# Performance work log

Hardware: AMD Instinct MI355X
Metric: run time of the kernel (lower is better)

The kernel has to match this reference:

```python
import jax, jax.numpy as jnp
import numpy as np

NUM_HEADS = 16
HIDDEN = 1024
HEAD = HIDDEN // NUM_HEADS


def setup_inputs() -> dict:
    key = jax.random.key(0)
    k1, k2, k3, k4, k5 = jax.random.split(key, 5)
    b, s, d = 2, 2048, HIDDEN
    scale = 1.0 / np.sqrt(d)
    return {
        "features": jax.random.normal(k1, (b, s, d), dtype=jnp.float32),
        "qkv_w": jax.random.normal(k2, (3 * d, d), dtype=jnp.float32) * scale,  # torch Linear weight [out,in]
        "qkv_b": jax.random.normal(k3, (3 * d,), dtype=jnp.float32) * 0.01,
        "out_w": jax.random.normal(k4, (d, d), dtype=jnp.float32) * scale,
        "out_b": jax.random.normal(k5, (d,), dtype=jnp.float32) * 0.01,
        "use_causal_mask": 0,
    }


def reference(features, qkv_w, qkv_b, out_w, out_b, use_causal_mask):
    b, s, d = features.shape
    qkv = features @ qkv_w.T + qkv_b                      # [b,s,3d]
    q, k, v = jnp.split(qkv, 3, axis=-1)
    # [b,s,d] -> [b,h,s,hd]
    def heads(x):
        return x.reshape(b, s, NUM_HEADS, HEAD).transpose(0, 2, 1, 3)
    q, k, v = heads(q), heads(k), heads(v)
    scores = jnp.einsum("bhqd,bhkd->bhqk", q, k) / np.sqrt(HEAD)
    if use_causal_mask:
        mask = jnp.triu(jnp.ones((s, s), dtype=bool), k=1)
        scores = jnp.where(mask, -jnp.inf, scores)
    attn = jax.nn.softmax(scores, axis=-1)
    out = jnp.einsum("bhqk,bhkd->bhqd", attn, v)          # [b,h,s,hd]
    out = out.transpose(0, 2, 1, 3).reshape(b, s, d)
    return out @ out_w.T + out_b
```

## Files before the change

kernel.cpp:

```cpp
#include <hip/hip_runtime.h>
#include <hip/hip_bf16.h>
#include <math.h>

#define BATCH 2
#define SEQ   2048
#define HID   1024
#define NHEAD 16
#define ROWS  (BATCH*SEQ)
#define QK_N  2048
#define VT_N  (BATCH*SEQ)

#define Q_SCALE 0.18033688011112042f

typedef __attribute__((ext_vector_type(8))) short bf16x8;
typedef __attribute__((ext_vector_type(4))) float f32x4;

__device__ __forceinline__ unsigned short f2b(float f) {
    unsigned u = __float_as_uint(f);
    u += 0x7FFF + ((u >> 16) & 1);
    return (unsigned short)(u >> 16);
}
__device__ __forceinline__ unsigned pk2c(float a, float b) {
    __hip_bfloat162 h = __float22bfloat162_rn(float2{a, b});
    union { __hip_bfloat162 h2; unsigned u; } cv; cv.h2 = h;
    return cv.u;
}

#define GLOAD_LDS16(gp, lp) \
    __builtin_amdgcn_global_load_lds((const __attribute__((address_space(1))) void*)(gp), \
                                     (__attribute__((address_space(3))) void*)(lp), 16, 0, 0)

__global__ __launch_bounds__(256)
void cvt_all(const float* __restrict__ a, unsigned short* __restrict__ oa, int na4,
             const float* __restrict__ b, unsigned short* __restrict__ ob, int nb4,
             const float* __restrict__ c, unsigned short* __restrict__ oc, int nc4) {
    const int total = na4 + nb4 + nc4;
    const int stride = gridDim.x * 256;
    for (int i = blockIdx.x * 256 + threadIdx.x; i < total; i += stride) {
        const float* src; unsigned short* dst; int j;
        if (i < na4)            { src = a; dst = oa; j = i; }
        else if (i < na4 + nb4) { src = b; dst = ob; j = i - na4; }
        else                    { src = c; dst = oc; j = i - na4 - nb4; }
        float4 v = reinterpret_cast<const float4*>(src)[j];
        ushort4 o;
        o.x = f2b(v.x); o.y = f2b(v.y); o.z = f2b(v.z); o.w = f2b(v.w);
        reinterpret_cast<ushort4*>(dst)[j] = o;
    }
}

__global__ __launch_bounds__(256)
void proj_fused(const unsigned short* __restrict__ fbf,
                const unsigned short* __restrict__ wbf,
                const float* __restrict__ qkv_b,
                unsigned short* __restrict__ qkbf,
                unsigned short* __restrict__ vtD) {
    __shared__ __align__(16) unsigned short As[128 * 32];
    __shared__ __align__(16) unsigned short Bs[128 * 32];
    const int tid = threadIdx.x;
    const int w = tid >> 6, l = tid & 63;
    const int wm = w >> 1, wn = w & 1;
    const int l15 = l & 15, l4 = l >> 4;

    const int bx = blockIdx.x;
    const bool isQK = bx < 512;
    const unsigned short* A;
    const unsigned short* Bm;
    long row0, col0;
    if (isQK) {
        row0 = (long)(bx >> 4) * 128;
        col0 = (long)(bx & 15) * 128;
        A = fbf;  Bm = wbf;
    } else {
        int r = bx - 512;
        row0 = (long)(r >> 5) * 128;
        col0 = (long)(r & 31) * 128;
        A = wbf + (size_t)2048 * 1024;
        Bm = fbf;
    }

    f32x4 acc[4][4];
    #pragma unroll
    for (int m = 0; m < 4; ++m)
        #pragma unroll
        for (int n = 0; n < 4; ++n) acc[m][n] = (f32x4)0.0f;

    const int lr   = l >> 2;
    const int slot = (l & 3) ^ (lr & 3);

    for (int k0 = 0; k0 < HID; k0 += 32) {
        __syncthreads();
        #pragma unroll
        for (int c = 0; c < 2; ++c) {
            int r = w * 32 + c * 16 + lr;
            GLOAD_LDS16(A  + (row0 + r) * HID + k0 + slot * 8, As + (w * 32 + c * 16) * 32);
            GLOAD_LDS16(Bm + (col0 + r) * HID + k0 + slot * 8, Bs + (w * 32 + c * 16) * 32);
        }
        __syncthreads();

        bf16x8 af[4], bfr[4];
        #pragma unroll
        for (int m = 0; m < 4; ++m) {
            int row = wm * 64 + m * 16 + l15;
            af[m] = *(const bf16x8*)((const char*)As + row * 64 + ((l4 ^ (row & 3)) << 4));
        }
        #pragma unroll
        for (int n = 0; n < 4; ++n) {
            int row = wn * 64 + n * 16 + l15;
            bfr[n] = *(const bf16x8*)((const char*)Bs + row * 64 + ((l4 ^ (row & 3)) << 4));
        }
        #pragma unroll
        for (int m = 0; m < 4; ++m)
            #pragma unroll
            for (int n = 0; n < 4; ++n)
                acc[m][n] = __builtin_amdgcn_mfma_f32_16x16x32_bf16(af[m], bfr[n], acc[m][n], 0, 0, 0);
    }

    #pragma unroll
    for (int m = 0; m < 4; ++m) {
        #pragma unroll
        for (int n = 0; n < 4; ++n) {
            long ccol = col0 + wn * 64 + n * 16 + l15;
            #pragma unroll
            for (int r2 = 0; r2 < 4; ++r2) {
                long crow = row0 + wm * 64 + m * 16 + l4 * 4 + r2;
                if (isQK) {
                    float v = acc[m][n][r2] + qkv_b[ccol];
                    qkbf[crow * QK_N + ccol] = (ccol < 1024) ? f2b(v * Q_SCALE) : f2b(v);
                } else {
                    float v = acc[m][n][r2] + qkv_b[2048 + crow];
                    vtD[crow * VT_N + ccol] = f2b(v);
                }
            }
        }
    }
}

__global__ __launch_bounds__(256)
void gemm_out(const unsigned short* __restrict__ A, const unsigned short* __restrict__ B,
              const float* __restrict__ bias, float* __restrict__ Cout,
              int M, int N, int K) {
    __shared__ __align__(16) unsigned short As[128 * 32];
    __shared__ __align__(16) unsigned short Bs[64 * 32];
    const int tid = threadIdx.x;
    const int w = tid >> 6, l = tid & 63;
    const int wm = w >> 1, wn = w & 1;
    const int l15 = l & 15, l4 = l >> 4;
    const long row0 = (long)blockIdx.y * 128;
    const long col0 = (long)blockIdx.x * 64;

    f32x4 acc[4][2];
    #pragma unroll
    for (int m = 0; m < 4; ++m)
        #pragma unroll
        for (int n = 0; n < 2; ++n) acc[m][n] = (f32x4)0.0f;

    const int lr   = l >> 2;
    const int slot = (l & 3) ^ (lr & 3);

    for (int k0 = 0; k0 < K; k0 += 32) {
        __syncthreads();
        #pragma unroll
        for (int c = 0; c < 2; ++c) {
            int r = w * 32 + c * 16 + lr;
            GLOAD_LDS16(A + (row0 + r) * K + k0 + slot * 8, As + (w * 32 + c * 16) * 32);
        }
        {
            int r = w * 16 + lr;
            GLOAD_LDS16(B + (col0 + r) * K + k0 + slot * 8, Bs + (w * 16) * 32);
        }
        __syncthreads();

        bf16x8 af[4], bfr[2];
        #pragma unroll
        for (int m = 0; m < 4; ++m) {
            int row = wm * 64 + m * 16 + l15;
            af[m] = *(const bf16x8*)((const char*)As + row * 64 + ((l4 ^ (row & 3)) << 4));
        }
        #pragma unroll
        for (int n = 0; n < 2; ++n) {
            int row = wn * 32 + n * 16 + l15;
            bfr[n] = *(const bf16x8*)((const char*)Bs + row * 64 + ((l4 ^ (row & 3)) << 4));
        }
        #pragma unroll
        for (int m = 0; m < 4; ++m)
            #pragma unroll
            for (int n = 0; n < 2; ++n)
                acc[m][n] = __builtin_amdgcn_mfma_f32_16x16x32_bf16(af[m], bfr[n], acc[m][n], 0, 0, 0);
    }

    #pragma unroll
    for (int m = 0; m < 4; ++m) {
        #pragma unroll
        for (int n = 0; n < 2; ++n) {
            long ccol = col0 + wn * 32 + n * 16 + l15;
            float bv = bias[ccol];
            #pragma unroll
            for (int r2 = 0; r2 < 4; ++r2) {
                long crow = row0 + wm * 64 + m * 16 + l4 * 4 + r2;
                Cout[crow * N + ccol] = acc[m][n][r2] + bv;
            }
        }
    }
}

__global__ __launch_bounds__(256, 4)
void attn_mfma(const unsigned short* __restrict__ qk, const unsigned short* __restrict__ vtD,
               unsigned short* __restrict__ attno, const int* __restrict__ use_mask) {
    __shared__ __align__(16) unsigned short Ks [64 * 64];
    __shared__ __align__(16) unsigned short Vts[64 * 64];
    __shared__ __align__(16) unsigned short Ps [4][32 * 40];
    const int tid = threadIdx.x;
    const int w = tid >> 6, l = tid & 63;
    const int l15 = l & 15, l4 = l >> 4;
    const int bid  = blockIdx.x;
    const int orig = (bid & 7) * 128 + (bid >> 3);
    const int qt = orig & 31, bh = orig >> 5;
    const int b = bh >> 4, h = bh & 15;
    const int q0 = qt * 64;
    const int qh = w & 1, kh = w >> 1;
    const int wq0 = q0 + qh * 32;
    const int causal = use_mask[0];
    const int NT = causal ? (qt + 1) : (SEQ / 64);

    bf16x8 qf[2][2];
    #pragma unroll
    for (int m = 0; m < 2; ++m) {
        const unsigned short* qp = qk + (size_t)(b * SEQ + wq0 + m * 16 + l15) * QK_N + h * 64;
        qf[m][0] = *(const bf16x8*)(qp + l4 * 8);
        qf[m][1] = *(const bf16x8*)(qp + 32 + l4 * 8);
    }

    f32x4 o_acc[2][4];
    #pragma unroll
    for (int m = 0; m < 2; ++m)
        #pragma unroll
        for (int n = 0; n < 4; ++n) o_acc[m][n] = (f32x4)0.0f;
    f32x4 l_acc[2] = {(f32x4)0.0f, (f32x4)0.0f};

    bf16x8 ones;
    #pragma unroll
    for (int j = 0; j < 8; ++j) ones[j] = (short)0x3F80;

    const int srow = l >> 3, g = l & 7;
    const int r0   = w * 16 + srow;
    const int wso  = (g ^ srow) << 3;
    unsigned short* pw = Ps[w];

    const unsigned short* kp = qk + (size_t)b * SEQ * QK_N + 1024 + h * 64
                                  + (size_t)r0 * QK_N + g * 8;
    const unsigned short* vp = vtD + (size_t)(h * 64 + r0) * VT_N + b * SEQ + g * 8;

    bf16x8 kreg[2], vreg[2];
    kreg[0] = *(const bf16x8*)(kp);
    kreg[1] = *(const bf16x8*)(kp + 8 * QK_N);
    vreg[0] = *(const bf16x8*)(vp);
    vreg[1] = *(const bf16x8*)(vp + 8 * VT_N);
    kp += (size_t)64 * QK_N;
    vp += 64;

    for (int kt = 0; kt < NT; ++kt) {
        __syncthreads();
        #pragma unroll
        for (int c = 0; c < 2; ++c) {
            *(bf16x8*)(Ks  + (r0 + c * 8) * 64 + wso) = kreg[c];
            *(bf16x8*)(Vts + (r0 + c * 8) * 64 + wso) = vreg[c];
        }
        __syncthreads();

        if (kt + 1 < NT) {
            kreg[0] = *(const bf16x8*)(kp);
            kreg[1] = *(const bf16x8*)(kp + 8 * QK_N);
            vreg[0] = *(const bf16x8*)(vp);
            vreg[1] = *(const bf16x8*)(vp + 8 * VT_N);
            kp += (size_t)64 * QK_N;
            vp += 64;
        }

        f32x4 s_acc[2][2];
        #pragma unroll
        for (int n2 = 0; n2 < 2; ++n2)
            #pragma unroll
            for (int m = 0; m < 2; ++m) s_acc[n2][m] = (f32x4)0.0f;
        __builtin_amdgcn_s_setprio(1);
        #pragma unroll
        for (int ks = 0; ks < 2; ++ks) {
            #pragma unroll
            for (int n2 = 0; n2 < 2; ++n2) {
                int row = kh * 32 + n2 * 16 + l15;
                bf16x8 kf = *(const bf16x8*)((const char*)Ks + row * 128 + (((ks * 4 + l4) ^ (row & 7)) << 4));
                #pragma unroll
                for (int m = 0; m < 2; ++m)
                    s_acc[n2][m] = __builtin_amdgcn_mfma_f32_16x16x32_bf16(kf, qf[m][ks], s_acc[n2][m], 0, 0, 0);
            }
        }
        __builtin_amdgcn_s_setprio(0);

        if (causal) {
            int kk0 = kt * 64 + kh * 32;
            #pragma unroll
            for (int n2 = 0; n2 < 2; ++n2)
                #pragma unroll
                for (int m = 0; m < 2; ++m)
                    #pragma unroll
                    for (int r2 = 0; r2 < 4; ++r2) {
                        int krow = kk0 + n2 * 16 + l4 * 4 + r2;
                        int qcol = wq0 + m * 16 + l15;
                        if (krow > qcol) s_acc[n2][m][r2] = -INFINITY;
                    }
        }

        #pragma unroll
        for (int m = 0; m < 2; ++m) {
            int prow = m * 16 + l15;
            #pragma unroll
            for (int n2 = 0; n2 < 2; ++n2) {
                float p0 = __builtin_amdgcn_exp2f(s_acc[n2][m][0]);
                float p1 = __builtin_amdgcn_exp2f(s_acc[n2][m][1]);
                float p2 = __builtin_amdgcn_exp2f(s_acc[n2][m][2]);
                float p3 = __builtin_amdgcn_exp2f(s_acc[n2][m][3]);
                uint2 pk;
                pk.x = pk2c(p0, p1);
                pk.y = pk2c(p2, p3);
                *(uint2*)((char*)pw + prow * 80 + n2 * 32 + l4 * 8) = pk;
            }
        }

        __builtin_amdgcn_s_setprio(1);
        bf16x8 pf[2];
        #pragma unroll
        for (int m = 0; m < 2; ++m) {
            int prow = m * 16 + l15;
            pf[m] = *(const bf16x8*)((const char*)pw + prow * 80 + l4 * 16);
            l_acc[m] = __builtin_amdgcn_mfma_f32_16x16x32_bf16(pf[m], ones, l_acc[m], 0, 0, 0);
        }
        #pragma unroll
        for (int n = 0; n < 4; ++n) {
            int vrow = n * 16 + l15;
            bf16x8 vf = *(const bf16x8*)((const char*)Vts + vrow * 128 + (((kh * 4 + l4) ^ (vrow & 7)) << 4));
            #pragma unroll
            for (int m = 0; m < 2; ++m)
                o_acc[m][n] = __builtin_amdgcn_mfma_f32_16x16x32_bf16(pf[m], vf, o_acc[m][n], 0, 0, 0);
        }
        __builtin_amdgcn_s_setprio(0);
    }

    __syncthreads();
    float* mq = (float*)(qh ? Vts : Ks);
    float* lb = (float*)&Ps[0][0];
    if (kh == 1) {
        #pragma unroll
        for (int m = 0; m < 2; ++m) {
            #pragma unroll
            for (int r2 = 0; r2 < 4; ++r2) {
                int qr = m * 16 + l4 * 4 + r2;
                #pragma unroll
                for (int n = 0; n < 4; ++n)
                    mq[qr * 64 + n * 16 + l15] = o_acc[m][n][r2];
                if (l15 == 0) lb[qh * 32 + qr] = l_acc[m][r2];
            }
        }
    }
    __syncthreads();
    if (kh == 0) {
        #pragma unroll
        for (int m = 0; m < 2; ++m) {
            #pragma unroll
            for (int r2 = 0; r2 < 4; ++r2) {
                int qr = m * 16 + l4 * 4 + r2;
                float lt = l_acc[m][r2] + lb[qh * 32 + qr];
                float inv = 1.0f / lt;
                size_t orow = (size_t)(b * SEQ + wq0 + qr);
                #pragma unroll
                for (int n = 0; n < 4; ++n) {
                    float o = o_acc[m][n][r2] + mq[qr * 64 + n * 16 + l15];
                    attno[orow * HID + h * 64 + n * 16 + l15] = f2b(o * inv);
                }
            }
        }
    }
}

extern "C" void kernel_launch(void* const* d_in, const int* in_sizes, int n_in,
                              void* d_out, int out_size, void* d_ws, size_t ws_size,
                              hipStream_t stream) {
    const float* features = (const float*)d_in[0];
    const float* qkv_w    = (const float*)d_in[1];
    const float* qkv_b    = (const float*)d_in[2];
    const float* out_w    = (const float*)d_in[3];
    const float* out_b    = (const float*)d_in[4];
    const int*   use_mask = (const int*)d_in[5];

    char* ws = (char*)d_ws;
    unsigned short* fbf     = (unsigned short*)(ws);
    unsigned short* wbf     = (unsigned short*)(ws + 8388608);
    unsigned short* owbf    = (unsigned short*)(ws + 14680064);
    unsigned short* qkbf    = (unsigned short*)(ws + 16777216);
    unsigned short* vtD     = (unsigned short*)(ws + 33554432);
    unsigned short* attnobf = (unsigned short*)(ws + 41943040);

    cvt_all<<<2048, 256, 0, stream>>>(features, fbf, 1048576,
                                      qkv_w, wbf, 786432,
                                      out_w, owbf, 262144);

    proj_fused<<<768, 256, 0, stream>>>(fbf, wbf, qkv_b, qkbf, vtD);

    attn_mfma<<<1024, 256, 0, stream>>>(qkbf, vtD, attnobf, use_mask);

    dim3 g3(HID / 64, ROWS / 128);
    gemm_out<<<g3, 256, 0, stream>>>(attnobf, owbf, out_b, (float*)d_out,
                                     ROWS, HID, HID);
}
```

Measured before the change: 130.5 us.

## Double-buffer LDS tiles in QKV projection GEMM to overlap loads with MFMA

Turns the projection GEMM's single-buffered K loop into a two-stage pipeline. Two LDS buffers per operand are used, and the global-to-LDS load for tile t+2 is issued while tile t is computed. Partial vmcnt waits and explicit barriers fence the stages. The goal is to hide global memory latency behind MFMA work. The cost is double the LDS footprint, which may lower occupancy, and the vmcnt count must exactly match the number of outstanding loads.

Measured after the change: 132.3 us. Within noise of the previous version (+1.4%).

```diff
diff --git a/kernel.cpp b/kernel.cpp
--- a/kernel.cpp
+++ b/kernel.cpp
@@ -54,8 +54,8 @@
                 const float* __restrict__ qkv_b,
                 unsigned short* __restrict__ qkbf,
                 unsigned short* __restrict__ vtD) {
-    __shared__ __align__(16) unsigned short As[128 * 32];
-    __shared__ __align__(16) unsigned short Bs[128 * 32];
+    __shared__ __align__(16) unsigned short As[2][128 * 32];
+    __shared__ __align__(16) unsigned short Bs[2][128 * 32];
     const int tid = threadIdx.x;
     const int w = tid >> 6, l = tid & 63;
     const int wm = w >> 1, wn = w & 1;
@@ -87,33 +87,68 @@
     const int lr   = l >> 2;
     const int slot = (l & 3) ^ (lr & 3);
 
-    for (int k0 = 0; k0 < HID; k0 += 32) {
-        __syncthreads();
-        #pragma unroll
-        for (int c = 0; c < 2; ++c) {
-            int r = w * 32 + c * 16 + lr;
-            GLOAD_LDS16(A  + (row0 + r) * HID + k0 + slot * 8, As + (w * 32 + c * 16) * 32);
-            GLOAD_LDS16(Bm + (col0 + r) * HID + k0 + slot * 8, Bs + (w * 32 + c * 16) * 32);
-        }
-        __syncthreads();
-
-        bf16x8 af[4], bfr[4];
-        #pragma unroll
-        for (int m = 0; m < 4; ++m) {
-            int row = wm * 64 + m * 16 + l15;
-            af[m] = *(const bf16x8*)((const char*)As + row * 64 + ((l4 ^ (row & 3)) << 4));
-        }
-        #pragma unroll
-        for (int n = 0; n < 4; ++n) {
-            int row = wn * 64 + n * 16 + l15;
-            bfr[n] = *(const bf16x8*)((const char*)Bs + row * 64 + ((l4 ^ (row & 3)) << 4));
-        }
-        #pragma unroll
-        for (int m = 0; m < 4; ++m)
-            #pragma unroll
-            for (int n = 0; n < 4; ++n)
-                acc[m][n] = __builtin_amdgcn_mfma_f32_16x16x32_bf16(af[m], bfr[n], acc[m][n], 0, 0, 0);
-    }
+#define PROJ_STAGE(T, BUF)                                                              \
+    {                                                                                   \
+        int kk = (T) * 32;                                                              \
+        _Pragma("unroll")                                                               \
+        for (int c = 0; c < 2; ++c) {                                                   \
+            int r = w * 32 + c * 16 + lr;                                               \
+            GLOAD_LDS16(A  + (row0 + r) * HID + kk + slot * 8,                          \
+                        As[BUF] + (w * 32 + c * 16) * 32);                              \
+            GLOAD_LDS16(Bm + (col0 + r) * HID + kk + slot * 8,                          \
+                        Bs[BUF] + (w * 32 + c * 16) * 32);                              \
+        }                                                                               \
+    }
+
+#define PROJ_COMPUTE(BUF)                                                               \
+    {                                                                                   \
+        bf16x8 af[4], bfr[4];                                                           \
+        _Pragma("unroll")                                                               \
+        for (int m = 0; m < 4; ++m) {                                                   \
+            int row = wm * 64 + m * 16 + l15;                                           \
+            af[m] = *(const bf16x8*)((const char*)As[BUF] + row * 64 +                  \
+                                     ((l4 ^ (row & 3)) << 4));                          \
+        }                                                                               \
+        _Pragma("unroll")                                                               \
+        for (int n = 0; n < 4; ++n) {                                                   \
+            int row = wn * 64 + n * 16 + l15;                                           \
+            bfr[n] = *(const bf16x8*)((const char*)Bs[BUF] + row * 64 +                 \
+                                      ((l4 ^ (row & 3)) << 4));                         \
+        }                                                                               \
+        _Pragma("unroll")                                                               \
+        for (int m = 0; m < 4; ++m)                                                     \
+            _Pragma("unroll")                                                           \
+            for (int n = 0; n < 4; ++n)                                                 \
+                acc[m][n] = __builtin_amdgcn_mfma_f32_16x16x32_bf16(af[m], bfr[n],      \
+                                                                    acc[m][n], 0, 0, 0);\
+    }
+
+    PROJ_STAGE(0, 0)
+    PROJ_STAGE(1, 1)
+
+    int cur = 0;
+    #pragma unroll 1
+    for (int t = 0; t < HID / 32 - 1; ++t) {
+        asm volatile("s_waitcnt vmcnt(4)" ::: "memory");
+        __builtin_amdgcn_sched_barrier(0);
+        __builtin_amdgcn_s_barrier();
+        __builtin_amdgcn_sched_barrier(0);
+
+        PROJ_COMPUTE(cur)
+
+        __builtin_amdgcn_sched_barrier(0);
+        __builtin_amdgcn_s_barrier();
+        __builtin_amdgcn_sched_barrier(0);
+        if (t + 2 < HID / 32) PROJ_STAGE(t + 2, cur)
+        cur ^= 1;
+    }
+    asm volatile("s_waitcnt vmcnt(0)" ::: "memory");
+    __builtin_amdgcn_sched_barrier(0);
+    __builtin_amdgcn_s_barrier();
+    __builtin_amdgcn_sched_barrier(0);
+    PROJ_COMPUTE(cur)
+#undef PROJ_STAGE
+#undef PROJ_COMPUTE
 
     #pragma unroll
     for (int m = 0; m < 4; ++m) {
```
